# Kernel tuning notes

Hardware: AMD Instinct MI355X
Metric: run time of the kernel (lower is better)

The kernel has to match this reference:

```python
import jax, jax.numpy as jnp
import numpy as np

N, C, T, V = 32, 96, 256, 25
S, REL, OUT, BC, KS = 3, 12, 96, 24, 5
DILS = (1, 2)


def setup_inputs() -> dict:
    key = jax.random.key(0)
    ks = jax.random.split(key, 32)
    rn = lambda i, sh, s=1.0: jax.random.normal(ks[i], sh, dtype=jnp.float32) * s
    ru = lambda i, sh: jax.random.uniform(ks[i], sh, dtype=jnp.float32, minval=0.5, maxval=1.5)
    return dict(
        x=rn(0, (N, C, T, V)),
        spd_A=rn(1, (V, V), 0.1),
        A3=rn(2, (S, V, V), 0.1),
        A6=rn(3, (6, V, V), 0.1),
        alpha=jnp.array([0.5], jnp.float32),
        beta=jnp.array([0.5], jnp.float32),
        gamma=jnp.array([0.5], jnp.float32),
        c1_w=rn(4, (S, REL, C), 0.1), c1_b=rn(5, (S, REL), 0.1),
        c2_w=rn(6, (S, REL, C), 0.1), c2_b=rn(7, (S, REL), 0.1),
        c4_w=rn(8, (S, OUT, REL), 0.1), c4_b=rn(9, (S, OUT), 0.1),
        c3_w=rn(10, (S, OUT, C), 0.1), c3_b=rn(11, (S, OUT), 0.1),
        gbn_s=ru(12, (OUT,)), gbn_b=rn(13, (OUT,), 0.1),
        pw_w=rn(14, (4, BC, OUT), 0.1), pw_b=rn(15, (4, BC), 0.1),
        pwbn_s=ru(16, (4, BC)), pwbn_b=rn(17, (4, BC), 0.1),
        tc_w=rn(18, (2, BC, BC, KS), 0.1), tc_b=rn(19, (2, BC), 0.1),
        tcbn_s=ru(20, (2, BC)), tcbn_b=rn(21, (2, BC), 0.1),
        mpbn_s=ru(22, (BC,)), mpbn_b=rn(23, (BC,), 0.1),
    )


def _bn4(h, s, b):  # eval-mode BN folded to per-channel scale/shift, h: [N,C,T,V]
    return h * s[None, :, None, None] + b[None, :, None, None]


def reference(x, spd_A, A3, A6, alpha, beta, gamma,
              c1_w, c1_b, c2_w, c2_b, c4_w, c4_b, c3_w, c3_b,
              gbn_s, gbn_b, pw_w, pw_b, pwbn_s, pwbn_b,
              tc_w, tc_b, tcbn_s, tcbn_b, mpbn_s, mpbn_b):
    # ---- unit_gcn with CTRGC relation modeling ----
    xm = x.mean(axis=2)                                           # [N,C,V] (1x1 conv commutes with T-mean)
    x1 = jnp.einsum('ncv,src->nsrv', xm, c1_w) + c1_b[None, :, :, None]
    x2 = jnp.einsum('ncv,src->nsrv', xm, c2_w) + c2_b[None, :, :, None]
    R = jnp.tanh(x1[..., :, None] - x2[..., None, :])             # [N,S,REL,V,V]
    M = jnp.einsum('nsruv,sor->nsouv', R, c4_w) + c4_b[None, :, :, None, None]
    A6_ex = jnp.tile(A6, (OUT // 6, 1, 1))                        # [OUT,V,V]; A6_ex[c] = A6[c % 6]
    A_at = (M * alpha[0] + A3[None, :, None] + A6_ex[None, None] * beta[0]
            + spd_A * gamma[0])                                   # [N,S,OUT,V,V]
    y = jnp.zeros((N, OUT, T, V), x.dtype)
    for s_ in range(S):
        x3 = jnp.einsum('nctv,oc->notv', x, c3_w[s_]) + c3_b[s_][None, :, None, None]
        y = y + jnp.einsum('nouv,notv->notu', A_at[:, s_], x3)
    y = jax.nn.relu(_bn4(y, gbn_s, gbn_b) + x)                    # residual down = identity (in==out)
    # ---- MultiScale_TemporalConv (internal residual=False) ----
    outs = []
    for b in range(2):  # dilated temporal branches
        h = jax.nn.relu(_bn4(jnp.einsum('nctv,oc->notv', y, pw_w[b])
                             + pw_b[b][None, :, None, None], pwbn_s[b], pwbn_b[b]))
        d = DILS[b]
        pad = 2 * d  # (KS + (KS-1)*(d-1) - 1)//2 for KS=5
        h = jax.lax.conv_general_dilated(
            h, tc_w[b][..., None], window_strides=(1, 1),
            padding=[(pad, pad), (0, 0)], rhs_dilation=(d, 1),
            dimension_numbers=('NCHW', 'OIHW', 'NCHW')) + tc_b[b][None, :, None, None]
        outs.append(_bn4(h, tcbn_s[b], tcbn_b[b]))
    # max-pool branch
    h = jax.nn.relu(_bn4(jnp.einsum('nctv,oc->notv', y, pw_w[2])
                         + pw_b[2][None, :, None, None], pwbn_s[2], pwbn_b[2]))
    h = jax.lax.reduce_window(h, -jnp.inf, jax.lax.max, (1, 1, 3, 1), (1, 1, 1, 1),
                              [(0, 0), (0, 0), (1, 1), (0, 0)])
    outs.append(_bn4(h, mpbn_s, mpbn_b))
    # plain 1x1 branch
    h = jnp.einsum('nctv,oc->notv', y, pw_w[3]) + pw_b[3][None, :, None, None]
    outs.append(_bn4(h, pwbn_s[3], pwbn_b[3]))
    out = jnp.concatenate(outs, axis=1)                           # [N,OUT,T,V]
    return jax.nn.relu(out + x)                                   # outer residual = identity
```

## Files before the change

### kernel.cpp

```cpp
#include <hip/hip_runtime.h>
#include <hip/hip_bf16.h>

typedef __hip_bfloat16 bf16;

#define NN 32
#define CC 96
#define TT 256
#define VV 25
#define SS 3
#define RR 12
#define OO 96
#define BCC 24
#define TV (TT*VV)
#define VV2 (VV*VV)

__device__ __forceinline__ float b2f(bf16 v){ return __bfloat162float(v); }
__device__ __forceinline__ bf16  f2b(float v){ return __float2bfloat16(v); }
__device__ __forceinline__ float u2f(unsigned short b){
    union{unsigned u; float f;} a; a.u = ((unsigned)b)<<16; return a.f;
}

__global__ __launch_bounds__(256) void k_mean(const float* __restrict__ x, float* __restrict__ xm)
{
    int idx = blockIdx.x*256 + threadIdx.x;
    if (idx >= NN*CC*VV) return;
    int v  = idx % VV;
    int nc = idx / VV;
    const float* p = x + (size_t)nc*TV + v;
    float s = 0.f;
    for (int t=0;t<TT;t++) s += p[t*VV];
    xm[idx] = s * (1.0f/TT);
}

__global__ __launch_bounds__(256) void k_aat(
    const float* __restrict__ xm,
    const float* __restrict__ c1_w, const float* __restrict__ c1_b,
    const float* __restrict__ c2_w, const float* __restrict__ c2_b,
    const float* __restrict__ c4_w, const float* __restrict__ c4_b,
    const float* __restrict__ A3,  const float* __restrict__ A6, const float* __restrict__ spd,
    const float* __restrict__ alpha, const float* __restrict__ beta, const float* __restrict__ gamma,
    float* __restrict__ Aat)
{
    __shared__ float s_xm[CC*VV];
    __shared__ float s_x1[RR*VV], s_x2[RR*VV];
    __shared__ float s_R[RR*VV2];
    __shared__ float s_c4[OO*RR];
    __shared__ float s_A3[VV2], s_spd[VV2];
    int n = blockIdx.x / SS, s = blockIdx.x % SS;
    int tid = threadIdx.x;
    for (int i=tid;i<CC*VV;i+=256) s_xm[i] = xm[(size_t)n*CC*VV + i];
    for (int i=tid;i<OO*RR;i+=256) s_c4[i] = c4_w[s*OO*RR + i];
    for (int i=tid;i<VV2;i+=256){ s_A3[i]=A3[s*VV2+i]; s_spd[i]=spd[i]; }
    __syncthreads();
    for (int i=tid;i<RR*VV;i+=256){
        int r=i/VV, u=i-r*VV;
        float a1=0.f, a2=0.f;
        for (int c=0;c<CC;c++){
            float xv = s_xm[c*VV+u];
            a1 += c1_w[(s*RR+r)*CC+c]*xv;
            a2 += c2_w[(s*RR+r)*CC+c]*xv;
        }
        s_x1[i]=a1+c1_b[s*RR+r];
        s_x2[i]=a2+c2_b[s*RR+r];
    }
    __syncthreads();
    for (int i=tid;i<RR*VV2;i+=256){
        int r=i/VV2, uv=i-r*VV2, u=uv/VV, v=uv-u*VV;
        s_R[i] = tanhf(s_x1[r*VV+u]-s_x2[r*VV+v]);
    }
    __syncthreads();
    float al=alpha[0], be=beta[0], ga=gamma[0];
    float* op = Aat + ((size_t)n*SS+s)*OO*VV2;
    for (int i=tid;i<OO*VV2;i+=256){
        int o=i/VV2, uv=i-o*VV2;
        float m=0.f;
        #pragma unroll
        for (int r=0;r<RR;r++) m += s_c4[o*RR+r]*s_R[r*VV2+uv];
        m += c4_b[s*OO+o];
        op[i] = m*al + s_A3[uv] + A6[(o%6)*VV2+uv]*be + s_spd[uv]*ga;
    }
}

__global__ __launch_bounds__(256,2) void k_gcn(
    const float* __restrict__ x, const float* __restrict__ c3_w, const float* __restrict__ c3_b,
    const float* __restrict__ Aat, const float* __restrict__ gbn_s, const float* __restrict__ gbn_b,
    float* __restrict__ y)
{
    __shared__ __align__(16) float s_w[CC*16];
    __shared__ float s_cb[12];
    __shared__ __align__(16) float s_x3[12*896];
    int bi = blockIdx.x;
    int og  = bi % 24;
    int tcb = (bi/24) & 7;
    int n   = bi / 192;
    int t0  = tcb*32;
    int tid = threadIdx.x;

    for (int i=tid;i<CC*12;i+=256){
        int c=i/12, k=i-c*12, s=k>>2, op=k&3;
        s_w[c*16+k] = c3_w[(s*OO + og*4+op)*CC + c];
    }
    if (tid<12){ int s=tid>>2, op=tid&3; s_cb[tid] = c3_b[s*OO + og*4+op]; }
    __syncthreads();

    float acc[4][12];
    #pragma unroll
    for (int j=0;j<4;j++)
        #pragma unroll
        for (int k=0;k<12;k++) acc[j][k]=0.f;
    size_t xb = (size_t)n*CC*TV + (size_t)t0*VV;
    int p3 = (tid<32) ? (768+tid) : 799;
    for (int c=0;c<CC;c++){
        float wv[12];
        *(float4*)&wv[0] = *(const float4*)&s_w[c*16];
        *(float4*)&wv[4] = *(const float4*)&s_w[c*16+4];
        *(float4*)&wv[8] = *(const float4*)&s_w[c*16+8];
        const float* xc = x + xb + (size_t)c*TV;
        float xv[4];
        xv[0]=xc[tid]; xv[1]=xc[tid+256]; xv[2]=xc[tid+512]; xv[3]=xc[p3];
        #pragma unroll
        for (int j=0;j<4;j++)
            #pragma unroll
            for (int k=0;k<12;k++) acc[j][k] += wv[k]*xv[j];
    }
    #pragma unroll
    for (int j=0;j<4;j++){
        int p = (j<3) ? (tid + j*256) : p3;
        bool wr = (j<3) || (tid<32);
        if (wr){
            int tc=p/25, v=p-tc*25;
            #pragma unroll
            for (int k=0;k<12;k++) s_x3[k*896 + tc*28 + v] = acc[j][k] + s_cb[k];
        }
    }
    __syncthreads();

    int w  = tid >> 6;
    int L  = tid & 63;
    int u  = L & 31;
    int th = L >> 5;
    int o  = og*4 + w;
    int u_eff = (u<VV)?u:(VV-1);
    float areg[75];
    #pragma unroll
    for (int s=0;s<3;s++){
        const float* Ap = Aat + (((size_t)n*SS+s)*OO + o)*VV2 + (size_t)u_eff*VV;
        #pragma unroll
        for (int v=0;v<25;v++) areg[s*25+v] = Ap[v];
    }
    float gs = gbn_s[o], gb = gbn_b[o];
    for (int ti=0; ti<16; ti++){
        int tl = ti*2 + th;
        float a2 = 0.f;
        #pragma unroll
        for (int s=0;s<3;s++){
            const float* xr = &s_x3[(s*4+w)*896 + tl*28];
            #pragma unroll
            for (int vc=0; vc<6; vc++){
                float4 xv4 = *(const float4*)(xr + vc*4);
                a2 += xv4.x*areg[s*25+vc*4]   + xv4.y*areg[s*25+vc*4+1]
                    + xv4.z*areg[s*25+vc*4+2] + xv4.w*areg[s*25+vc*4+3];
            }
            a2 += xr[24]*areg[s*25+24];
        }
        if (u < VV){
            int t = t0 + tl;
            size_t oix = ((size_t)(n*OO+o)*TT + t)*VV + u;
            float yv = gs*a2 + gb + x[oix];
            y[oix] = yv>0.f?yv:0.f;
        }
    }
}

__global__ __launch_bounds__(256,2) void k_pw_h(
    const float* __restrict__ yws, const float* __restrict__ pw_w, const float* __restrict__ pw_b,
    const float* __restrict__ pwbn_s, const float* __restrict__ pwbn_b,
    bf16* __restrict__ h1)
{
    __shared__ __align__(16) float s_w[OO*BCC];
    __shared__ float s_sc[BCC], s_sh[BCC];
    int b   = blockIdx.x/160;
    int rem = blockIdx.x - b*160;
    int n   = rem/5;
    int chunk = rem - (rem/5)*5;
    int pbase = chunk*256 + threadIdx.x;
    for (int i=threadIdx.x;i<OO*BCC;i+=256){
        int o=i/BCC, cp=i-o*BCC;
        s_w[i] = pw_w[(b*BCC+cp)*OO + o];
    }
    if (threadIdx.x<BCC){
        int cp=threadIdx.x;
        float sc = pwbn_s[b*BCC+cp];
        s_sc[cp]=sc;
        s_sh[cp]= sc*pw_b[b*BCC+cp] + pwbn_b[b*BCC+cp];
    }
    __syncthreads();
    float acc[5][BCC];
    #pragma unroll
    for (int j=0;j<5;j++)
        #pragma unroll
        for (int i=0;i<BCC;i++) acc[j][i]=0.f;
    const float* yp = yws + (size_t)n*OO*TV + pbase;
    for (int o=0;o<OO;o++){
        float wv[BCC];
        #pragma unroll
        for (int q=0;q<6;q++) *(float4*)&wv[q*4] = *(const float4*)&s_w[o*BCC + q*4];
        float yv[5];
        #pragma unroll
        for (int j=0;j<5;j++) yv[j] = yp[(size_t)o*TV + j*1280];
        #pragma unroll
        for (int j=0;j<5;j++)
            #pragma unroll
            for (int cp=0;cp<BCC;cp++) acc[j][cp] += wv[cp]*yv[j];
    }
    size_t hb = ((size_t)(b*NN+n)*BCC)*TV + pbase;
    #pragma unroll
    for (int j=0;j<5;j++)
        #pragma unroll
        for (int cp=0;cp<BCC;cp++){
            float h = s_sc[cp]*acc[j][cp] + s_sh[cp];
            h1[hb + (size_t)cp*TV + j*1280] = f2b(h>0.f?h:0.f);
        }
}

__global__ __launch_bounds__(256,2) void k_pw3(
    float* yout, const float* __restrict__ pw_w, const float* __restrict__ pw_b,
    const float* __restrict__ pwbn_s, const float* __restrict__ pwbn_b,
    const float* __restrict__ x)
{
    __shared__ __align__(16) float s_w[OO*BCC];
    __shared__ float s_sc[BCC], s_sh[BCC];
    const int b = 3;
    int n   = blockIdx.x/5;
    int chunk = blockIdx.x - n*5;
    int pbase = chunk*256 + threadIdx.x;
    for (int i=threadIdx.x;i<OO*BCC;i+=256){
        int o=i/BCC, cp=i-o*BCC;
        s_w[i] = pw_w[(b*BCC+cp)*OO + o];
    }
    if (threadIdx.x<BCC){
        int cp=threadIdx.x;
        float sc = pwbn_s[b*BCC+cp];
        s_sc[cp]=sc;
        s_sh[cp]= sc*pw_b[b*BCC+cp] + pwbn_b[b*BCC+cp];
    }
    __syncthreads();
    float acc[5][BCC];
    #pragma unroll
    for (int j=0;j<5;j++)
        #pragma unroll
        for (int i=0;i<BCC;i++) acc[j][i]=0.f;
    const float* yp = yout + (size_t)n*OO*TV + pbase;
    for (int o=0;o<OO;o++){
        float wv[BCC];
        #pragma unroll
        for (int q=0;q<6;q++) *(float4*)&wv[q*4] = *(const float4*)&s_w[o*BCC + q*4];
        float yv[5];
        #pragma unroll
        for (int j=0;j<5;j++) yv[j] = yp[(size_t)o*TV + j*1280];
        #pragma unroll
        for (int j=0;j<5;j++)
            #pragma unroll
            for (int cp=0;cp<BCC;cp++) acc[j][cp] += wv[cp]*yv[j];
    }
    size_t ob = ((size_t)n*OO + 72)*TV + pbase;
    #pragma unroll
    for (int j=0;j<5;j++)
        #pragma unroll
        for (int cp=0;cp<BCC;cp++){
            float h = s_sc[cp]*acc[j][cp] + s_sh[cp];
            size_t ix = ob + (size_t)cp*TV + j*1280;
            float r = h + x[ix];
            yout[ix] = r>0.f?r:0.f;
        }
}

template<int D>
__device__ __forceinline__ void tcn_conv(int n, int br, int t0, int t4, int v, int vv, bool act,
    const float* __restrict__ tc_w, const float* __restrict__ tc_b,
    const float* __restrict__ tcbn_s, const float* __restrict__ tcbn_b,
    const float* __restrict__ x, float* __restrict__ out, const unsigned short* s_h)
{
    const int W = 4 + 4*D;
    int tb = 4 + t4*4 - 2*D;
    for (int g=0; g<4; g++){
        float acc[6][4];
        #pragma unroll
        for (int cpi=0;cpi<6;cpi++)
            #pragma unroll
            for (int i=0;i<4;i++) acc[cpi][i]=0.f;
        for (int ci=0; ci<24; ci++){
            float win[W];
            #pragma unroll
            for (int j=0;j<W;j++) win[j] = u2f(s_h[(ci*40 + tb + j)*26 + vv]);
            #pragma unroll
            for (int cpi=0; cpi<6; cpi++){
                int cp = g*6+cpi;
                const float* wp = tc_w + ((br*BCC+cp)*BCC + ci)*5;
                float w0=wp[0],w1=wp[1],w2=wp[2],w3=wp[3],w4=wp[4];
                #pragma unroll
                for (int i=0;i<4;i++)
                    acc[cpi][i] += w0*win[i] + w1*win[i+D] + w2*win[i+2*D]
                                 + w3*win[i+3*D] + w4*win[i+4*D];
            }
        }
        if (act){
            #pragma unroll
            for (int cpi=0; cpi<6; cpi++){
                int ch = br*BCC + g*6+cpi;
                float tbias=tc_b[ch], ts=tcbn_s[ch], tb2=tcbn_b[ch];
                #pragma unroll
                for (int i=0;i<4;i++){
                    size_t oix = ((size_t)(n*OO+ch)*TT + (t0+t4*4+i))*VV + v;
                    float r = ts*(acc[cpi][i]+tbias) + tb2 + x[oix];
                    out[oix] = r>0.f?r:0.f;
                }
            }
        }
    }
}

__global__ __launch_bounds__(256,2) void k_tcn(
    const bf16* __restrict__ h1, const float* __restrict__ tc_w, const float* __restrict__ tc_b,
    const float* __restrict__ tcbn_s, const float* __restrict__ tcbn_b,
    const float* __restrict__ mpbn_s, const float* __restrict__ mpbn_b,
    const float* __restrict__ x, float* __restrict__ out)
{
    __shared__ unsigned short s_h[24*40*26];
    int bi  = blockIdx.x;
    int n   = bi / 24;
    int rem = bi % 24;
    int br  = rem >> 3;
    int tcb = rem & 7;
    int t0  = tcb*32;
    int tid = threadIdx.x;

    const unsigned short* hb = (const unsigned short*)(h1 + ((size_t)(br*NN+n)*BCC)*TV);
    unsigned short padv = (br==2) ? (unsigned short)0xFF80 : (unsigned short)0;
    for (int ci=0; ci<24; ci++){
        const unsigned short* hc = hb + (size_t)ci*TV;
        #pragma unroll
        for (int j=0;j<5;j++){
            int idx = j*256 + tid;
            if (idx < 1040){
                int tt = idx/26, v = idx - tt*26;
                int gt = t0 - 4 + tt;
                unsigned short bits = padv;
                if (v<25 && gt>=0 && gt<TT) bits = hc[gt*VV+v];
                s_h[(ci*40+tt)*26 + v] = bits;
            }
        }
    }
    __syncthreads();

    int t4 = tid>>5, v = tid&31;
    bool act = v<25;
    int vv = act ? v : 24;

    if (br==0){
        tcn_conv<1>(n,br,t0,t4,v,vv,act,tc_w,tc_b,tcbn_s,tcbn_b,x,out,s_h);
    } else if (br==1){
        tcn_conv<2>(n,br,t0,t4,v,vv,act,tc_w,tc_b,tcbn_s,tcbn_b,x,out,s_h);
    } else {
        int tb = 4 + t4*4 - 1;
        for (int cp=0; cp<24; cp++){
            float win[6];
            #pragma unroll
            for (int j=0;j<6;j++) win[j] = u2f(s_h[(cp*40 + tb + j)*26 + vv]);
            float ms=mpbn_s[cp], mb=mpbn_b[cp];
            if (act){
                #pragma unroll
                for (int i=0;i<4;i++){
                    float m = fmaxf(fmaxf(win[i],win[i+1]),win[i+2]);
                    size_t oix = ((size_t)(n*OO+(48+cp))*TT + (t0+t4*4+i))*VV + v;
                    float r = ms*m + mb + x[oix];
                    out[oix] = r>0.f?r:0.f;
                }
            }
        }
    }
}

extern "C" void kernel_launch(void* const* d_in, const int* in_sizes, int n_in,
                              void* d_out, int out_size, void* d_ws, size_t ws_size,
                              hipStream_t stream)
{
    const float* x     = (const float*)d_in[0];
    const float* spd   = (const float*)d_in[1];
    const float* A3    = (const float*)d_in[2];
    const float* A6    = (const float*)d_in[3];
    const float* alpha = (const float*)d_in[4];
    const float* beta  = (const float*)d_in[5];
    const float* gamma = (const float*)d_in[6];
    const float* c1_w  = (const float*)d_in[7];
    const float* c1_b  = (const float*)d_in[8];
    const float* c2_w  = (const float*)d_in[9];
    const float* c2_b  = (const float*)d_in[10];
    const float* c4_w  = (const float*)d_in[11];
    const float* c4_b  = (const float*)d_in[12];
    const float* c3_w  = (const float*)d_in[13];
    const float* c3_b  = (const float*)d_in[14];
    const float* gbn_s = (const float*)d_in[15];
    const float* gbn_b = (const float*)d_in[16];
    const float* pw_w  = (const float*)d_in[17];
    const float* pw_b  = (const float*)d_in[18];
    const float* pwbn_s= (const float*)d_in[19];
    const float* pwbn_b= (const float*)d_in[20];
    const float* tc_w  = (const float*)d_in[21];
    const float* tc_b  = (const float*)d_in[22];
    const float* tcbn_s= (const float*)d_in[23];
    const float* tcbn_b= (const float*)d_in[24];
    const float* mpbn_s= (const float*)d_in[25];
    const float* mpbn_b= (const float*)d_in[26];
    float* out = (float*)d_out;

    char* ws = (char*)d_ws;
    float* xm  = (float*)(ws);
    float* Aat = (float*)(ws + 307200);
    bf16*  h1  = (bf16*)(ws);

    k_mean<<<dim3(300), dim3(256), 0, stream>>>(x, xm);
    k_aat <<<dim3(96),  dim3(256), 0, stream>>>(xm, c1_w,c1_b,c2_w,c2_b,c4_w,c4_b,
                                                A3, A6, spd, alpha, beta, gamma, Aat);
    k_gcn <<<dim3(6144),dim3(256), 0, stream>>>(x, c3_w, c3_b, Aat, gbn_s, gbn_b, out);
    k_pw_h<<<dim3(480), dim3(256), 0, stream>>>(out, pw_w, pw_b, pwbn_s, pwbn_b, h1);
    k_pw3 <<<dim3(160), dim3(256), 0, stream>>>(out, pw_w, pw_b, pwbn_s, pwbn_b, x);
    k_tcn <<<dim3(768), dim3(256), 0, stream>>>(h1, tc_w, tc_b, tcbn_s, tcbn_b,
                                                mpbn_s, mpbn_b, x, out);
}
```

Before: 740.5 us.

## Compute c3 1x1 conv in k_gcn with fp16 MFMA via LDS-staged x tiles

Replaces the scalar FMA loop for the per-block 1x1 conv (12 output channels × 800 positions × 96 inputs) with 16x16x16 fp16 MFMA instructions. Input x is loaded as float4, converted to fp16 and staged in padded LDS in 16-channel chunks, and weights are staged in LDS as fp16 padded to 16 rows. This aims to cut VALU work, but it adds LDS traffic and syncs per chunk and lowers input precision to fp16.

After: 846.6 us. 14.3% more time.

```diff
diff --git a/kernel.cpp b/kernel.cpp
--- a/kernel.cpp
+++ b/kernel.cpp
@@ -2,6 +2,9 @@
 #include <hip/hip_bf16.h>
 
 typedef __hip_bfloat16 bf16;
+typedef __attribute__((ext_vector_type(4))) _Float16 half4;
+typedef __attribute__((ext_vector_type(2))) _Float16 half2v;
+typedef __attribute__((ext_vector_type(4))) float f32x4;
 
 #define NN 32
 #define CC 96
@@ -81,64 +84,97 @@
     }
 }
 
+#define XROW 20
 __global__ __launch_bounds__(256,2) void k_gcn(
     const float* __restrict__ x, const float* __restrict__ c3_w, const float* __restrict__ c3_b,
     const float* __restrict__ Aat, const float* __restrict__ gbn_s, const float* __restrict__ gbn_b,
     float* __restrict__ y)
 {
-    __shared__ __align__(16) float s_w[CC*16];
-    __shared__ float s_cb[12];
-    __shared__ __align__(16) float s_x3[12*896];
-    int bi = blockIdx.x;
+    __shared__ __align__(16) _Float16 s_x[800*XROW];
+    __shared__ __align__(16) float    s_x3[12*896];
+    __shared__ __align__(16) _Float16 s_w[6*16*16];
+    __shared__ float s_cb[16];
+
+    int bi  = blockIdx.x;
     int og  = bi % 24;
     int tcb = (bi/24) & 7;
     int n   = bi / 192;
     int t0  = tcb*32;
     int tid = threadIdx.x;
 
-    for (int i=tid;i<CC*12;i+=256){
-        int c=i/12, k=i-c*12, s=k>>2, op=k&3;
-        s_w[c*16+k] = c3_w[(s*OO + og*4+op)*CC + c];
-    }
-    if (tid<12){ int s=tid>>2, op=tid&3; s_cb[tid] = c3_b[s*OO + og*4+op]; }
-    __syncthreads();
-
-    float acc[4][12];
-    #pragma unroll
-    for (int j=0;j<4;j++)
-        #pragma unroll
-        for (int k=0;k<12;k++) acc[j][k]=0.f;
+    for (int i=tid;i<16*96;i+=256){
+        int m=i/96, c=i-m*96;
+        float wf = 0.f;
+        if (m<12){ int s=m>>2, op=m&3; wf = c3_w[(s*OO + og*4+op)*CC + c]; }
+        s_w[((c>>4)*16+m)*16 + (c&15)] = (_Float16)wf;
+    }
+    if (tid<16){
+        float b=0.f;
+        if (tid<12){ int s=tid>>2, op=tid&3; b = c3_b[s*OO + og*4+op]; }
+        s_cb[tid]=b;
+    }
+
+    int l  = tid & 63;
+    int li = l & 15, q = l >> 4;
+    int wv_id = tid >> 6;
+    int start = wv_id*13;
+    int cnt   = (wv_id<3) ? 13 : 11;
+
+    f32x4 acc[13];
+    #pragma unroll
+    for (int j=0;j<13;++j) acc[j] = (f32x4){0.f,0.f,0.f,0.f};
+
     size_t xb = (size_t)n*CC*TV + (size_t)t0*VV;
-    int p3 = (tid<32) ? (768+tid) : 799;
-    for (int c=0;c<CC;c++){
-        float wv[12];
-        *(float4*)&wv[0] = *(const float4*)&s_w[c*16];
-        *(float4*)&wv[4] = *(const float4*)&s_w[c*16+4];
-        *(float4*)&wv[8] = *(const float4*)&s_w[c*16+8];
-        const float* xc = x + xb + (size_t)c*TV;
-        float xv[4];
-        xv[0]=xc[tid]; xv[1]=xc[tid+256]; xv[2]=xc[tid+512]; xv[3]=xc[p3];
-        #pragma unroll
-        for (int j=0;j<4;j++)
-            #pragma unroll
-            for (int k=0;k<12;k++) acc[j][k] += wv[k]*xv[j];
-    }
-    #pragma unroll
-    for (int j=0;j<4;j++){
-        int p = (j<3) ? (tid + j*256) : p3;
-        bool wr = (j<3) || (tid<32);
-        if (wr){
-            int tc=p/25, v=p-tc*25;
-            #pragma unroll
-            for (int k=0;k<12;k++) s_x3[k*896 + tc*28 + v] = acc[j][k] + s_cb[k];
-        }
-    }
-    __syncthreads();
-
-    int w  = tid >> 6;
-    int L  = tid & 63;
-    int u  = L & 31;
-    int th = L >> 5;
+    for (int ck=0; ck<6; ++ck){
+        __syncthreads();
+        int c0 = ck*16;
+        for (int it=0; it<7; ++it){
+            int task = tid + it*256;
+            if (task < 1600){
+                int cpair = task & 7;
+                int pq    = task >> 3;
+                const float* r0 = x + xb + (size_t)(c0 + cpair*2)*TV + pq*4;
+                float4 a = *(const float4*)r0;
+                float4 b = *(const float4*)(r0 + TV);
+                #pragma unroll
+                for (int ii=0; ii<4; ++ii){
+                    int p = pq*4 + ii;
+                    half2v hv;
+                    hv[0] = (_Float16)((&a.x)[ii]);
+                    hv[1] = (_Float16)((&b.x)[ii]);
+                    *(half2v*)&s_x[p*XROW + cpair*2] = hv;
+                }
+            }
+        }
+        __syncthreads();
+        half4 a4 = *(const half4*)(s_w + (ck*16+li)*16 + q*4);
+        #pragma unroll
+        for (int j=0;j<13;++j){
+            if (j < cnt){
+                half4 b4 = *(const half4*)(s_x + ((start+j)*16 + li)*XROW + q*4);
+                acc[j] = __builtin_amdgcn_mfma_f32_16x16x16f16(a4, b4, acc[j], 0, 0, 0);
+            }
+        }
+    }
+
+    if (q < 3){
+        #pragma unroll
+        for (int j=0;j<13;++j){
+            if (j < cnt){
+                int p = (start+j)*16 + li;
+                int t = p/25, v = p - t*25;
+                float* dst = s_x3 + (q*4)*896 + t*28 + v;
+                #pragma unroll
+                for (int r=0;r<4;++r)
+                    dst[r*896] = acc[j][r] + s_cb[q*4+r];
+            }
+        }
+    }
+    __syncthreads();
+
+    int w  = wv_id;
+    int u  = l & 31;
+    int th = l >> 5;
     int o  = og*4 + w;
     int u_eff = (u<VV)?u:(VV-1);
     float areg[75];
```
